# Kernel tuning notes

Measured on AMD Instinct MI355X. Metric: run time of the kernel, lower is better.

## Reference

```python
import jax, jax.numpy as jnp
import numpy as np

HIDDEN = 64
INPUT_DIM = 128
DEMO_DIM = 12
ATT_WIDTH = 1e7  # history_only=True, attention_width=None -> causal


def setup_inputs() -> dict:
    key = jax.random.key(0)
    ks = jax.random.split(key, 8)
    B, T = 4, 512
    inp = {
        "input": jax.random.normal(ks[0], (B, T, INPUT_DIM), dtype=jnp.float32),
        "demo": jax.random.normal(ks[1], (B, DEMO_DIM), dtype=jnp.float32),
        "Wt": jax.random.normal(ks[2], (INPUT_DIM, HIDDEN), dtype=jnp.float32) * 0.08,
        "Wx": jax.random.normal(ks[3], (INPUT_DIM, HIDDEN), dtype=jnp.float32) * 0.08,
        "Wd": jax.random.normal(ks[4], (DEMO_DIM, HIDDEN), dtype=jnp.float32) * 0.25,
        "bh": jnp.zeros((HIDDEN,), dtype=jnp.float32),
        "Wa": jax.random.normal(ks[5], (HIDDEN, 1), dtype=jnp.float32) * 0.12,
        "ba": jnp.zeros((1,), dtype=jnp.float32),
    }
    return inp


def reference(input, demo, Wt, Wx, Wd, bh, Wa, ba):
    B, T, D = input.shape
    # additive attention scores via broadcasted [B,T,T,H] intermediate
    q = (input @ Wt)[:, :, None, :]          # [B,T,1,H]
    k = (input @ Wx)[:, None, :, :]          # [B,1,T,H]
    d = (demo @ Wd)[:, None, None, :]        # [B,1,1,H]
    h = jnp.tanh(q + k + d + bh)             # [B,T,T,H]
    e = (h @ Wa)[..., 0] + ba[0]             # [B,T,T]
    # custom softmax: exp(e - rowmax) BEFORE masking, then mask, then normalize
    e = jnp.exp(e - jnp.max(e, axis=-1, keepdims=True))
    idx = jnp.arange(T, dtype=jnp.float32)
    lower = idx[:, None] - (ATT_WIDTH - 1.0)  # history_only
    upper = lower + ATT_WIDTH
    mask = ((lower <= idx[None, :]) & (idx[None, :] < upper)).astype(e.dtype)
    e = e * mask
    s = jnp.sum(e, axis=-1, keepdims=True)
    e = e / (s + 1e-7)
    v = jnp.einsum('bts,bsd->btd', e, input)  # [B,T,D]
    return (v, e)
```

## Files before the change

### kernel.cpp

```cpp
#include <hip/hip_runtime.h>
#include <math.h>

#define B_ 4
#define T_ 512
#define D_ 128
#define H_ 64
#define DEMO_ 12
#define LOG2E 1.4426950408889634f
#define SC2   (2.0f * LOG2E)

typedef float float4v __attribute__((ext_vector_type(4)));
typedef float float2v __attribute__((ext_vector_type(2)));

__global__ __launch_bounds__(256) void prep_kernel(
    const float* __restrict__ input, const float* __restrict__ demo,
    const float* __restrict__ Wt, const float* __restrict__ Wx,
    const float* __restrict__ Wd, const float* __restrict__ bh,
    float* __restrict__ Q, float* __restrict__ K2T)
{
    __shared__ float in_sh[8 * D_];
    int tid  = threadIdx.x;
    int row0 = blockIdx.x * 8;
    int b    = row0 >> 9;

    #pragma unroll
    for (int k = 0; k < 4; ++k)
        in_sh[tid + 256 * k] = input[row0 * D_ + tid + 256 * k];
    __syncthreads();

    int h  = tid & 63;
    int rr = tid >> 6;

    float dB = bh[h];
    #pragma unroll
    for (int kk = 0; kk < DEMO_; ++kk)
        dB = fmaf(demo[b * DEMO_ + kk], Wd[kk * H_ + h], dB);

    float q0 = 0.f, q1 = 0.f, x0 = 0.f, x1 = 0.f;
    #pragma unroll 8
    for (int k = 0; k < D_; ++k) {
        float wt = Wt[k * H_ + h];
        float wx = Wx[k * H_ + h];
        float a0 = in_sh[rr * D_ + k];
        float a1 = in_sh[(rr + 4) * D_ + k];
        q0 = fmaf(a0, wt, q0);
        q1 = fmaf(a1, wt, q1);
        x0 = fmaf(a0, wx, x0);
        x1 = fmaf(a1, wx, x1);
    }

    int ra = row0 + rr, rb = row0 + rr + 4;
    Q[ra * H_ + h] = q0 * SC2;
    Q[rb * H_ + h] = q1 * SC2;
    int ta = ra & (T_ - 1), tb = rb & (T_ - 1);
    K2T[(b * H_ + h) * T_ + ta] = (x0 + dB) * SC2;
    K2T[(b * H_ + h) * T_ + tb] = (x1 + dB) * SC2;
}

__global__ __launch_bounds__(1024, 8) void attn_kernel(
    const float* __restrict__ input,
    const float* __restrict__ Qs, const float* __restrict__ K2T,
    const float* __restrict__ Wa, const float* __restrict__ ba,
    float* __restrict__ out_v, float* __restrict__ out_e)
{
    __shared__ float qsh[H_ * 4];
    __shared__ float red_m[16 * 2];
    __shared__ float red_s[16 * 2];
    __shared__ float csh;
    __shared__ float p_sh[T_ * 4];
    __shared__ float partial[8][4 * D_];

    int tid  = threadIdx.x;
    int b    = blockIdx.y;
    int i0   = blockIdx.x * 4;
    int lane = tid & 63, wv = tid >> 6;
    int j    = tid & (T_ - 1);
    int u    = tid >> 9;
    int g0   = 2 * u;

    if (tid < 256) {
        int h = tid >> 2, g = tid & 3;
        qsh[tid] = Qs[(size_t)(b * T_ + i0 + g) * H_ + h];
    }
    if (tid < 64) {
        float w = Wa[tid];
        #pragma unroll
        for (int off = 32; off; off >>= 1) w += __shfl_down(w, off, 64);
        if (tid == 0) csh = (ba[0] + w) * LOG2E;
    }
    __syncthreads();

    const float* k2p = K2T + (size_t)b * H_ * T_ + j;

    float acc0 = 0.f, acc1 = 0.f;
    #pragma unroll 2
    for (int h0 = 0; h0 < H_; h0 += 8) {
        float kv[8];
        #pragma unroll
        for (int uu = 0; uu < 8; ++uu)
            kv[uu] = k2p[(size_t)(h0 + uu) * T_];
        #pragma unroll
        for (int uu = 0; uu < 8; ++uu) {
            int h    = h0 + uu;
            float wa = Wa[h];
            float2v q2 = *(const float2v*)&qsh[h * 4 + g0];
            float ex0 = __builtin_amdgcn_exp2f(q2[0] + kv[uu]);
            float ex1 = __builtin_amdgcn_exp2f(q2[1] + kv[uu]);
            acc0 = fmaf(wa, __builtin_amdgcn_rcpf(1.0f + ex0), acc0);
            acc1 = fmaf(wa, __builtin_amdgcn_rcpf(1.0f + ex1), acc1);
        }
    }

    float CL  = csh;
    float eg0 = fmaf(-2.0f * LOG2E, acc0, CL);
    float eg1 = fmaf(-2.0f * LOG2E, acc1, CL);

    float M0 = eg0, M1 = eg1;
    #pragma unroll
    for (int off = 32; off; off >>= 1) {
        M0 = fmaxf(M0, __shfl_down(M0, off, 64));
        M1 = fmaxf(M1, __shfl_down(M1, off, 64));
    }
    if (lane == 0) ((float2v*)red_m)[wv] = (float2v){M0, M1};
    __syncthreads();
    {
        float2v m = ((float2v*)red_m)[u * 8];
        #pragma unroll
        for (int w = 1; w < 8; ++w) {
            float2v mw = ((float2v*)red_m)[u * 8 + w];
            m[0] = fmaxf(m[0], mw[0]);
            m[1] = fmaxf(m[1], mw[1]);
        }
        M0 = m[0]; M1 = m[1];
    }

    float p0 = __builtin_amdgcn_exp2f(eg0 - M0);
    float p1 = __builtin_amdgcn_exp2f(eg1 - M1);
    if (j > i0 + g0)     p0 = 0.0f;
    if (j > i0 + g0 + 1) p1 = 0.0f;
    *(float2v*)&p_sh[j * 4 + g0] = (float2v){p0, p1};
    float S0 = p0, S1 = p1;
    #pragma unroll
    for (int off = 32; off; off >>= 1) {
        S0 += __shfl_down(S0, off, 64);
        S1 += __shfl_down(S1, off, 64);
    }
    if (lane == 0) ((float2v*)red_s)[wv] = (float2v){S0, S1};
    __syncthreads();

    float inv4[4];
    {
        float2v a = ((float2v*)red_s)[0];
        float2v c = ((float2v*)red_s)[8];
        #pragma unroll
        for (int w = 1; w < 8; ++w) {
            float2v aw = ((float2v*)red_s)[w];
            float2v cw = ((float2v*)red_s)[8 + w];
            a[0] += aw[0]; a[1] += aw[1];
            c[0] += cw[0]; c[1] += cw[1];
        }
        inv4[0] = __builtin_amdgcn_rcpf(a[0] + 1e-7f);
        inv4[1] = __builtin_amdgcn_rcpf(a[1] + 1e-7f);
        inv4[2] = __builtin_amdgcn_rcpf(c[0] + 1e-7f);
        inv4[3] = __builtin_amdgcn_rcpf(c[1] + 1e-7f);
    }

    out_e[((size_t)(b * T_ + i0 + g0))     * T_ + j] = p0 * inv4[g0];
    out_e[((size_t)(b * T_ + i0 + g0 + 1)) * T_ + j] = p1 * inv4[g0 + 1];

    {
        int d  = tid & 127;
        int s8 = tid >> 7;
        const float* inp = input + ((size_t)(b * T_) + s8 * 64) * D_ + d;
        float va[4] = {0.f, 0.f, 0.f, 0.f};
        #pragma unroll 4
        for (int jj = 0; jj < 64; ++jj) {
            float x = inp[(size_t)jj * D_];
            float4v p4 = *(const float4v*)&p_sh[(s8 * 64 + jj) * 4];
            #pragma unroll
            for (int g = 0; g < 4; ++g) va[g] = fmaf(p4[g], x, va[g]);
        }
        #pragma unroll
        for (int g = 0; g < 4; ++g)
            partial[s8][g * D_ + d] = va[g] * inv4[g];
    }
    __syncthreads();

    if (tid < 512) {
        int g  = tid >> 7;
        int dd = tid & 127;
        float v = 0.f;
        #pragma unroll
        for (int s = 0; s < 8; ++s) v += partial[s][g * D_ + dd];
        out_v[(size_t)(b * T_ + i0 + g) * D_ + dd] = v;
    }
}

extern "C" void kernel_launch(void* const* d_in, const int* in_sizes, int n_in,
                              void* d_out, int out_size, void* d_ws, size_t ws_size,
                              hipStream_t stream)
{
    const float* input = (const float*)d_in[0];
    const float* demo  = (const float*)d_in[1];
    const float* Wt    = (const float*)d_in[2];
    const float* Wx    = (const float*)d_in[3];
    const float* Wd    = (const float*)d_in[4];
    const float* bh    = (const float*)d_in[5];
    const float* Wa    = (const float*)d_in[6];
    const float* ba    = (const float*)d_in[7];

    float* out_v = (float*)d_out;
    float* out_e = out_v + (size_t)B_ * T_ * D_;

    float* Q   = (float*)d_ws;
    float* K2T = Q + (size_t)B_ * T_ * H_;

    prep_kernel<<<dim3(B_ * T_ / 8), 256, 0, stream>>>(input, demo, Wt, Wx, Wd, bh, Q, K2T);
    attn_kernel<<<dim3(T_ / 4, B_), 1024, 0, stream>>>(input, Q, K2T, Wa, ba, out_v, out_e);
}
```

Before: 99.16 us.

## Skip masked causal tiles and use two-row 512-thread attention blocks

The attention kernel now handles two query rows per 512-thread block instead of four rows per 1024-thread block. Wavefronts whose key columns lie entirely above the causal diagonal skip the tanh-score computation, and PV slices past the diagonal skip their input loads. Block indices are interleaved so early and late rows mix across the grid, which balances the uneven causal work. The Wa-sum constant moves into the prep kernel and is written to workspace, and the per-row normalisation is applied at the final output store.

```diff
diff --git a/kernel.cpp b/kernel.cpp
--- a/kernel.cpp
+++ b/kernel.cpp
@@ -9,14 +9,14 @@
 #define LOG2E 1.4426950408889634f
 #define SC2   (2.0f * LOG2E)
 
-typedef float float4v __attribute__((ext_vector_type(4)));
 typedef float float2v __attribute__((ext_vector_type(2)));
 
 __global__ __launch_bounds__(256) void prep_kernel(
     const float* __restrict__ input, const float* __restrict__ demo,
     const float* __restrict__ Wt, const float* __restrict__ Wx,
     const float* __restrict__ Wd, const float* __restrict__ bh,
-    float* __restrict__ Q, float* __restrict__ K2T)
+    const float* __restrict__ Wa, const float* __restrict__ ba,
+    float* __restrict__ Q, float* __restrict__ K2T, float* __restrict__ Cs)
 {
     __shared__ float in_sh[8 * D_];
     int tid  = threadIdx.x;
@@ -55,65 +55,61 @@
     int ta = ra & (T_ - 1), tb = rb & (T_ - 1);
     K2T[(b * H_ + h) * T_ + ta] = (x0 + dB) * SC2;
     K2T[(b * H_ + h) * T_ + tb] = (x1 + dB) * SC2;
-}
-
-__global__ __launch_bounds__(1024, 8) void attn_kernel(
-    const float* __restrict__ input,
-    const float* __restrict__ Qs, const float* __restrict__ K2T,
-    const float* __restrict__ Wa, const float* __restrict__ ba,
-    float* __restrict__ out_v, float* __restrict__ out_e)
-{
-    __shared__ float qsh[H_ * 4];
-    __shared__ float red_m[16 * 2];
-    __shared__ float red_s[16 * 2];
-    __shared__ float csh;
-    __shared__ float p_sh[T_ * 4];
-    __shared__ float partial[8][4 * D_];
-
-    int tid  = threadIdx.x;
-    int b    = blockIdx.y;
-    int i0   = blockIdx.x * 4;
-    int lane = tid & 63, wv = tid >> 6;
-    int j    = tid & (T_ - 1);
-    int u    = tid >> 9;
-    int g0   = 2 * u;
-
-    if (tid < 256) {
-        int h = tid >> 2, g = tid & 3;
-        qsh[tid] = Qs[(size_t)(b * T_ + i0 + g) * H_ + h];
-    }
-    if (tid < 64) {
+
+    if (blockIdx.x == 0 && tid < 64) {
         float w = Wa[tid];
         #pragma unroll
         for (int off = 32; off; off >>= 1) w += __shfl_down(w, off, 64);
-        if (tid == 0) csh = (ba[0] + w) * LOG2E;
-    }
-    __syncthreads();
-
+        if (tid == 0) Cs[0] = (ba[0] + w) * LOG2E;
+    }
+}
+
+__global__ __launch_bounds__(512, 8) void attn_kernel(
+    const float* __restrict__ input,
+    const float* __restrict__ Qs, const float* __restrict__ K2T,
+    const float* __restrict__ Wa, const float* __restrict__ Cs,
+    float* __restrict__ out_v, float* __restrict__ out_e)
+{
+    __shared__ float p_sh[T_ * 2];
+    __shared__ float red_m[8 * 2];
+    __shared__ float red_s[8 * 2];
+    __shared__ float partial[4][2 * D_];
+
+    int tid  = threadIdx.x;
+    int bx   = blockIdx.x;
+    int b    = blockIdx.y;
+    int y    = ((bx & 7) << 5) | (bx >> 3);
+    int i0   = 2 * y, i1 = i0 + 1;
+    int lane = tid & 63, wv = tid >> 6;
+    int j    = tid;
+
+    const float* qr0 = Qs + (size_t)(b * T_ + i0) * H_;
+    const float* qr1 = qr0 + H_;
     const float* k2p = K2T + (size_t)b * H_ * T_ + j;
-
-    float acc0 = 0.f, acc1 = 0.f;
-    #pragma unroll 2
-    for (int h0 = 0; h0 < H_; h0 += 8) {
-        float kv[8];
-        #pragma unroll
-        for (int uu = 0; uu < 8; ++uu)
-            kv[uu] = k2p[(size_t)(h0 + uu) * T_];
-        #pragma unroll
-        for (int uu = 0; uu < 8; ++uu) {
-            int h    = h0 + uu;
-            float wa = Wa[h];
-            float2v q2 = *(const float2v*)&qsh[h * 4 + g0];
-            float ex0 = __builtin_amdgcn_exp2f(q2[0] + kv[uu]);
-            float ex1 = __builtin_amdgcn_exp2f(q2[1] + kv[uu]);
-            acc0 = fmaf(wa, __builtin_amdgcn_rcpf(1.0f + ex0), acc0);
-            acc1 = fmaf(wa, __builtin_amdgcn_rcpf(1.0f + ex1), acc1);
-        }
-    }
-
-    float CL  = csh;
-    float eg0 = fmaf(-2.0f * LOG2E, acc0, CL);
-    float eg1 = fmaf(-2.0f * LOG2E, acc1, CL);
+    float CL = Cs[0];
+
+    float eg0 = -INFINITY, eg1 = -INFINITY;
+    if ((wv << 6) <= i1) {
+        float acc0 = 0.f, acc1 = 0.f;
+        #pragma unroll 2
+        for (int h0 = 0; h0 < H_; h0 += 8) {
+            float kv[8];
+            #pragma unroll
+            for (int u = 0; u < 8; ++u)
+                kv[u] = k2p[(size_t)(h0 + u) * T_];
+            #pragma unroll
+            for (int u = 0; u < 8; ++u) {
+                float wa = Wa[h0 + u];
+                float q0 = qr0[h0 + u], q1 = qr1[h0 + u];
+                float ex0 = __builtin_amdgcn_exp2f(q0 + kv[u]);
+                float ex1 = __builtin_amdgcn_exp2f(q1 + kv[u]);
+                acc0 = fmaf(wa, __builtin_amdgcn_rcpf(1.0f + ex0), acc0);
+                acc1 = fmaf(wa, __builtin_amdgcn_rcpf(1.0f + ex1), acc1);
+            }
+        }
+        if (j <= i0) eg0 = fmaf(-2.0f * LOG2E, acc0, CL);
+        if (j <= i1) eg1 = fmaf(-2.0f * LOG2E, acc1, CL);
+    }
 
     float M0 = eg0, M1 = eg1;
     #pragma unroll
@@ -124,21 +120,19 @@
     if (lane == 0) ((float2v*)red_m)[wv] = (float2v){M0, M1};
     __syncthreads();
     {
-        float2v m = ((float2v*)red_m)[u * 8];
+        float2v m = ((float2v*)red_m)[0];
         #pragma unroll
         for (int w = 1; w < 8; ++w) {
-            float2v mw = ((float2v*)red_m)[u * 8 + w];
+            float2v mw = ((float2v*)red_m)[w];
             m[0] = fmaxf(m[0], mw[0]);
             m[1] = fmaxf(m[1], mw[1]);
         }
         M0 = m[0]; M1 = m[1];
     }
 
-    float p0 = __builtin_amdgcn_exp2f(eg0 - M0);
-    float p1 = __builtin_amdgcn_exp2f(eg1 - M1);
-    if (j > i0 + g0)     p0 = 0.0f;
-    if (j > i0 + g0 + 1) p1 = 0.0f;
-    *(float2v*)&p_sh[j * 4 + g0] = (float2v){p0, p1};
+    float p0 = (j <= i0) ? __builtin_amdgcn_exp2f(eg0 - M0) : 0.0f;
+    float p1 = (j <= i1) ? __builtin_amdgcn_exp2f(eg1 - M1) : 0.0f;
+    *(float2v*)&p_sh[j * 2] = (float2v){p0, p1};
     float S0 = p0, S1 = p1;
     #pragma unroll
     for (int off = 32; off; off >>= 1) {
@@ -148,51 +142,48 @@
     if (lane == 0) ((float2v*)red_s)[wv] = (float2v){S0, S1};
     __syncthreads();
 
-    float inv4[4];
+    float inv0, inv1;
     {
-        float2v a = ((float2v*)red_s)[0];
-        float2v c = ((float2v*)red_s)[8];
+        float2v s = ((float2v*)red_s)[0];
         #pragma unroll
         for (int w = 1; w < 8; ++w) {
-            float2v aw = ((float2v*)red_s)[w];
-            float2v cw = ((float2v*)red_s)[8 + w];
-            a[0] += aw[0]; a[1] += aw[1];
-            c[0] += cw[0]; c[1] += cw[1];
-        }
-        inv4[0] = __builtin_amdgcn_rcpf(a[0] + 1e-7f);
-        inv4[1] = __builtin_amdgcn_rcpf(a[1] + 1e-7f);
-        inv4[2] = __builtin_amdgcn_rcpf(c[0] + 1e-7f);
-        inv4[3] = __builtin_amdgcn_rcpf(c[1] + 1e-7f);
-    }
-
-    out_e[((size_t)(b * T_ + i0 + g0))     * T_ + j] = p0 * inv4[g0];
-    out_e[((size_t)(b * T_ + i0 + g0 + 1)) * T_ + j] = p1 * inv4[g0 + 1];
+            float2v sw = ((float2v*)red_s)[w];
+            s[0] += sw[0]; s[1] += sw[1];
+        }
+        inv0 = __builtin_amdgcn_rcpf(s[0] + 1e-7f);
+        inv1 = __builtin_amdgcn_rcpf(s[1] + 1e-7f);
+    }
+
+    out_e[((size_t)(b * T_ + i0)) * T_ + j] = p0 * inv0;
+    out_e[((size_t)(b * T_ + i1)) * T_ + j] = p1 * inv1;
 
     {
         int d  = tid & 127;
-        int s8 = tid >> 7;
-        const float* inp = input + ((size_t)(b * T_) + s8 * 64) * D_ + d;
-        float va[4] = {0.f, 0.f, 0.f, 0.f};
-        #pragma unroll 4
-        for (int jj = 0; jj < 64; ++jj) {
-            float x = inp[(size_t)jj * D_];
-            float4v p4 = *(const float4v*)&p_sh[(s8 * 64 + jj) * 4];
-            #pragma unroll
-            for (int g = 0; g < 4; ++g) va[g] = fmaf(p4[g], x, va[g]);
-        }
-        #pragma unroll
-        for (int g = 0; g < 4; ++g)
-            partial[s8][g * D_ + d] = va[g] * inv4[g];
-    }
-    __syncthreads();
-
-    if (tid < 512) {
-        int g  = tid >> 7;
+        int s4 = tid >> 7;
+        float va0 = 0.f, va1 = 0.f;
+        if ((s4 << 7) <= i1) {
+            const float* inp = input + ((size_t)(b * T_) + (s4 << 7)) * D_ + d;
+            const float* pp  = p_sh + (s4 << 7) * 2;
+            #pragma unroll 4
+            for (int jj = 0; jj < 128; ++jj) {
+                float x = inp[(size_t)jj * D_];
+                float2v p2 = *(const float2v*)&pp[jj * 2];
+                va0 = fmaf(p2[0], x, va0);
+                va1 = fmaf(p2[1], x, va1);
+            }
+        }
+        partial[s4][d]      = va0;
+        partial[s4][D_ + d] = va1;
+    }
+    __syncthreads();
+
+    if (tid < 256) {
+        int r  = tid >> 7;
         int dd = tid & 127;
-        float v = 0.f;
-        #pragma unroll
-        for (int s = 0; s < 8; ++s) v += partial[s][g * D_ + dd];
-        out_v[(size_t)(b * T_ + i0 + g) * D_ + dd] = v;
+        float v = partial[0][r * D_ + dd] + partial[1][r * D_ + dd]
+                + partial[2][r * D_ + dd] + partial[3][r * D_ + dd];
+        float inv = r ? inv1 : inv0;
+        out_v[(size_t)(b * T_ + i0 + r) * D_ + dd] = v * inv;
     }
 }
 
@@ -214,7 +205,9 @@
 
     float* Q   = (float*)d_ws;
     float* K2T = Q + (size_t)B_ * T_ * H_;
-
-    prep_kernel<<<dim3(B_ * T_ / 8), 256, 0, stream>>>(input, demo, Wt, Wx, Wd, bh, Q, K2T);
-    attn_kernel<<<dim3(T_ / 4, B_), 1024, 0, stream>>>(input, Q, K2T, Wa, ba, out_v, out_e);
+    float* Cs  = K2T + (size_t)B_ * H_ * T_;
+
+    prep_kernel<<<dim3(B_ * T_ / 8), 256, 0, stream>>>(input, demo, Wt, Wx, Wd, bh,
+                                                       Wa, ba, Q, K2T, Cs);
+    attn_kernel<<<dim3(256, B_), 512, 0, stream>>>(input, Q, K2T, Wa, Cs, out_v, out_e);
 }
```

Result: no change. 100.5 us (+1.3%).
